# Performance work log

Hardware: AMD Instinct MI355X
Metric: run time of the kernel (lower is better)

Reference implementation:

```python
import jax, jax.numpy as jnp
import numpy as np

GAIN_RELU = float(np.sqrt(2.0))  # torch.nn.init.calculate_gain('relu')
EPS = 1e-12  # F.normalize eps

N_NODES = 50000
N_EDGES = 1600000
IN_DIM = 8
HID = 32
EMB = 32


def setup_inputs() -> dict:
    key = jax.random.key(0)
    ks = jax.random.split(key, 20)
    x = jax.random.normal(ks[0], (N_NODES, IN_DIM), dtype=jnp.float32)
    edge_index = jax.random.randint(ks[1], (2, N_EDGES), 0, N_NODES, dtype=jnp.int64)
    d = {"x": x, "edge_index": edge_index}
    # Three WeBConv layers: (in->HID), (3*HID->HID), (3*HID->EMB)
    dims = [(IN_DIM, HID), (3 * HID, HID), (3 * HID, EMB)]
    ki = 2
    for li, (din, dout) in enumerate(dims, start=1):
        s = 1.0 / np.sqrt(din)  # torch Linear default init scale (uniform)
        d[f"w{li}_up"] = jax.random.uniform(ks[ki], (dout, din), jnp.float32, -s, s); ki += 1
        d[f"w{li}_down"] = jax.random.uniform(ks[ki], (dout, din), jnp.float32, -s, s); ki += 1
        d[f"w{li}_bias"] = jax.random.uniform(ks[ki], (dout, din), jnp.float32, -s, s); ki += 1
        d[f"ew{li}_up"] = jax.random.normal(ks[ki], (N_EDGES,), jnp.float32) * GAIN_RELU; ki += 1
        d[f"ew{li}_down"] = jax.random.normal(ks[ki], (N_EDGES,), jnp.float32) * GAIN_RELU; ki += 1
    return d


def _propagate(xp, src, dst, edge_weight, n_nodes):
    # degree-normalized (1/deg of target), edge-weighted scatter-add
    deg = jnp.zeros((n_nodes,), xp.dtype).at[dst].add(1.0)
    deg_inv = jnp.where(deg > 0, 1.0 / deg, 0.0)  # inf -> 0
    w = deg_inv[dst] * edge_weight  # [E]
    msgs = w[:, None] * xp[src]  # [E, F] gather + scale
    return jnp.zeros((n_nodes, xp.shape[1]), xp.dtype).at[dst].add(msgs)


def _webconv(x, edge_index, w_up, w_down, w_bias, ew_up, ew_down):
    n = x.shape[0]
    row, col = edge_index[0], edge_index[1]
    up_x = x @ w_up.T
    down_x = x @ w_down.T
    bias_x = x @ w_bias.T
    x_up = _propagate(up_x, row, col, ew_up, n)          # normal direction
    x_down = _propagate(down_x, col, row, ew_down, n)    # flipud(edge_index)
    cat = jnp.concatenate([x_up, x_down, bias_x], axis=-1)
    norm = jnp.maximum(jnp.linalg.norm(cat, axis=-1, keepdims=True), EPS)
    return cat / norm


def reference(x, edge_index,
              w1_up, w1_down, w1_bias, ew1_up, ew1_down,
              w2_up, w2_down, w2_bias, ew2_up, ew2_down,
              w3_up, w3_down, w3_bias, ew3_up, ew3_down):
    act = lambda h: jax.nn.leaky_relu(h, negative_slope=0.1)
    h = act(_webconv(x, edge_index, w1_up, w1_down, w1_bias, ew1_up, ew1_down))
    h = act(_webconv(h, edge_index, w2_up, w2_down, w2_bias, ew2_up, ew2_down))
    h = act(_webconv(h, edge_index, w3_up, w3_down, w3_bias, ew3_up, ew3_down))
    mean_up = (ew1_up + ew2_up + ew3_up) / 3.0
    mean_down = (ew1_down + ew2_down + ew3_down) / 3.0
    return h, mean_up, mean_down
```

## Files before the change

kernel.cpp:

```cpp
#include <hip/hip_runtime.h>
#include <hip/hip_bf16.h>
#include <math.h>

typedef __hip_bfloat16 bf16;
typedef unsigned short ushort_t;

#define NBMAX 1024
#define BSH 8
#define CH 3072
#define CSRCAP 6144

__device__ __forceinline__ float ldf(const void* p, long i, int isbf) {
    return isbf ? __bfloat162float(((const bf16*)p)[i]) : ((const float*)p)[i];
}
__device__ __forceinline__ int lde(const int* ei, int half, long e, long E, int is64) {
    long idx = half ? (E + e) : e;
    return is64 ? ei[idx * 2] : ei[idx];
}
__device__ __forceinline__ float u2f(ushort_t u) {
    union { unsigned int i; float f; } v; v.i = ((unsigned)u) << 16; return v.f;
}
__device__ __forceinline__ ushort_t f2u(float f) {
    bf16 h = __float2bfloat16(f);
    return *reinterpret_cast<ushort_t*>(&h);
}
__device__ __forceinline__ float lo2f(unsigned sp) {
    union { unsigned i; float f; } v; v.i = sp << 16; return v.f;
}
__device__ __forceinline__ float hi2f(unsigned sp) {
    union { unsigned i; float f; } v; v.i = sp & 0xffff0000u; return v.f;
}

struct DetectArgs {
    const void* p[16];
    long n[16];
    const int* ei;
    long E;
    int* flags;
};

__global__ void k_detect(DetectArgs a) {
    __shared__ int cnt;
    if (threadIdx.x == 0) cnt = 0;
    __syncthreads();
    int b = blockIdx.x;
    int bad = 0;
    if (b < 16) {
        const bf16* p = (const bf16*)a.p[b];
        long m = a.n[b] < 4096 ? a.n[b] : 4096;
        for (long i = threadIdx.x; i < m; i += 256) {
            float v = __bfloat162float(p[i]);
            if (!(fabsf(v) < 100.0f)) bad++;
        }
        atomicAdd(&cnt, bad);
        __syncthreads();
        if (threadIdx.x == 0) a.flags[b] = ((long)cnt * 16 < m) ? 1 : 0;
    } else {
        long m = a.E / 2 < 4096 ? a.E / 2 : 4096;
        for (long i = threadIdx.x; i < m; i += 256) {
            if (a.ei[2 * i + 1] != 0) bad++;
        }
        atomicAdd(&cnt, bad);
        __syncthreads();
        if (threadIdx.x == 0) a.flags[16] = (cnt < (int)(m / 16) + 1) ? 1 : 0;
    }
}


__global__ void kb_count(const int* __restrict__ ei, long E, const int* __restrict__ flags,
                         int NB, int* __restrict__ bc) {
    __shared__ int h0[NBMAX], h1[NBMAX];
    for (int i = threadIdx.x; i < NB; i += 256) { h0[i] = 0; h1[i] = 0; }
    __syncthreads();
    int is64 = flags[16];
    long base = (long)blockIdx.x * CH;
#pragma unroll
    for (int i = 0; i < CH / 256; i++) {
        long e = base + i * 256 + threadIdx.x;
        if (e < E) {
            int c = lde(ei, 1, e, E, is64);
            int r = lde(ei, 0, e, E, is64);
            atomicAdd(&h0[c >> BSH], 1);
            atomicAdd(&h1[r >> BSH], 1);
        }
    }
    __syncthreads();
    for (int i = threadIdx.x; i < NB; i += 256) {
        if (h0[i]) atomicAdd(&bc[i], h0[i]);
        if (h1[i]) atomicAdd(&bc[NBMAX + i], h1[i]);
    }
}

__global__ void kb_scan(const int* __restrict__ bc, int* __restrict__ bb,
                        int* __restrict__ gcur, int NB) {
    if (threadIdx.x < 2) {
        int dir = threadIdx.x;
        int acc = 0;
        for (int i = 0; i < NB; i++) { bb[dir * (NBMAX + 1) + i] = acc; acc += bc[dir * NBMAX + i]; }
        bb[dir * (NBMAX + 1) + NB] = acc;
    }
    __syncthreads();
    for (int i = threadIdx.x; i < 2 * NBMAX; i += blockDim.x) {
        int d = i / NBMAX, b = i - d * NBMAX;
        gcur[i] = bb[d * (NBMAX + 1) + (b < NB ? b : NB)];
    }
}

__global__ __launch_bounds__(512) void kb_fill(
                        const int* __restrict__ ei, long E, const int* __restrict__ flags,
                        int NB, int NBp, int* __restrict__ gcur,
                        const void* __restrict__ eu1, const void* __restrict__ eu2,
                        const void* __restrict__ eu3, const void* __restrict__ ed1,
                        const void* __restrict__ ed2, const void* __restrict__ ed3,
                        int2* __restrict__ bse_a, ushort_t* __restrict__ bse_w3) {
    extern __shared__ char dynlds[];
    int2* ssA      = (int2*)dynlds;
    ushort_t* ssW  = (ushort_t*)(ssA + CH);
    ushort_t* sbkt = ssW + CH;
    int* h    = (int*)(sbkt + CH);
    int* lofs = h + NBp;
    int* cur  = lofs + NBp;
    int* gb   = cur + NBp;
    int* sc   = gb + NBp;
    int tid = threadIdx.x;
    int dir = blockIdx.y;
    int is64 = flags[16];
    const void* w1p = dir ? ed1 : eu1;
    const void* w2p = dir ? ed2 : eu2;
    const void* w3p = dir ? ed3 : eu3;
    int f1 = flags[dir ? 5 : 4], f2 = flags[dir ? 10 : 9], f3 = flags[dir ? 15 : 14];
    for (int i = tid; i < NBp; i += 512) { h[i] = 0; cur[i] = 0; }
    __syncthreads();
    long base = (long)blockIdx.x * CH;
    const int EPT = CH / 512;
    int myd[EPT], mys[EPT], myw12[EPT];
    ushort_t myw3[EPT];
#pragma unroll
    for (int i = 0; i < EPT; i++) {
        long e = base + i * 512 + tid;
        myd[i] = -1;
        if (e < E) {
            myd[i] = lde(ei, dir ? 0 : 1, e, E, is64);
            mys[i] = lde(ei, dir ? 1 : 0, e, E, is64);
            myw12[i] = (unsigned)f2u(ldf(w1p, e, f1)) | ((unsigned)f2u(ldf(w2p, e, f2)) << 16);
            myw3[i] = f2u(ldf(w3p, e, f3));
            atomicAdd(&h[myd[i] >> BSH], 1);
        }
    }
    __syncthreads();
    int i0 = tid * 2;
    int a0 = (i0 < NBp) ? h[i0] : 0;
    int a1 = (i0 + 1 < NBp) ? h[i0 + 1] : 0;
    int ts = a0 + a1;
    sc[tid] = ts;
    __syncthreads();
    for (int d = 1; d < 512; d <<= 1) {
        int t = (tid >= d) ? sc[tid - d] : 0;
        __syncthreads();
        sc[tid] += t;
        __syncthreads();
    }
    int eb = sc[tid] - ts;
    if (i0 < NBp) lofs[i0] = eb;
    if (i0 + 1 < NBp) lofs[i0 + 1] = eb + a0;
    __syncthreads();
#pragma unroll
    for (int i = 0; i < EPT; i++) {
        if (myd[i] >= 0) {
            int b = myd[i] >> BSH;
            int r = atomicAdd(&cur[b], 1);
            int p = lofs[b] + r;
            ssA[p] = make_int2(mys[i] | ((myd[i] & 255) << 24), myw12[i]);
            ssW[p] = myw3[i];
            sbkt[p] = (ushort_t)b;
        }
    }
    __syncthreads();
    for (int b = tid; b < NB; b += 512) {
        int c = h[b];
        gb[b] = c ? atomicAdd(&gcur[dir * NBMAX + b], c) : 0;
    }
    __syncthreads();
    long rem = E - base;
    int nvalid = rem >= CH ? CH : (rem > 0 ? (int)rem : 0);
    int2* osA = bse_a + (long)dir * E;
    ushort_t* osW = bse_w3 + (long)dir * E;
    for (int s = tid; s < nvalid; s += 512) {
        int b = sbkt[s];
        long p = (long)gb[b] + (s - lofs[b]);
        osA[p] = ssA[s];
        osW[p] = ssW[s];
    }
}

__global__ __launch_bounds__(512) void kb_csr(
                       const int* __restrict__ bb, const int2* __restrict__ bse_a,
                       const ushort_t* __restrict__ bse_w3,
                       long E, int NB, long N,
                       int* __restrict__ off_c, int* __restrict__ off_r,
                       int* __restrict__ list_c, int* __restrict__ list_r,
                       ushort_t* __restrict__ wc6) {
    __shared__ int2 sA[CSRCAP];
    __shared__ ushort_t sW[CSRCAP];
    __shared__ int h[256], lofs[256], cur[256], sc[256];
    int tid = threadIdx.x;
    int b = blockIdx.x, dir = blockIdx.y;
    int base = bb[dir * (NBMAX + 1) + b];
    int cnt  = bb[dir * (NBMAX + 1) + b + 1] - base;
    const int2* bsA = bse_a + (long)dir * E;
    const ushort_t* bsW = bse_w3 + (long)dir * E;
    int* off  = dir ? off_r : off_c;
    int* list = dir ? list_r : list_c;
    ushort_t* o1 = wc6 + (long)(0 + dir) * E;
    ushort_t* o2 = wc6 + (long)(2 + dir) * E;
    ushort_t* o3 = wc6 + (long)(4 + dir) * E;
    if (tid < 256) { h[tid] = 0; cur[tid] = 0; }
    __syncthreads();
    int nb0 = b << BSH;
    for (int s = tid; s < cnt; s += 512)
        atomicAdd(&h[(unsigned)bsA[base + s].x >> 24], 1);
    __syncthreads();
    if (tid < 256) sc[tid] = h[tid];
    __syncthreads();
    for (int d = 1; d < 256; d <<= 1) {
        int t = 0;
        if (tid < 256 && tid >= d) t = sc[tid - d];
        __syncthreads();
        if (tid < 256) sc[tid] += t;
        __syncthreads();
    }
    if (tid < 256) lofs[tid] = sc[tid] - h[tid];
    __syncthreads();
    if (tid < 256) {
        long n = (long)nb0 + tid;
        if (n < N) off[n] = base + lofs[tid];
    }
    if (b == 0 && tid == 0) off[N] = (int)E;
    int mid = lofs[128];
    int cnt1 = cnt - mid;
    if (mid <= CSRCAP && cnt1 <= CSRCAP) {
        for (int s = tid; s < cnt; s += 512) {
            int2 se = bsA[base + s];
            int local = (unsigned)se.x >> 24;
            if (local < 128) {
                int r = atomicAdd(&cur[local], 1);
                int p = lofs[local] + r;
                sA[p] = se;
                sW[p] = bsW[base + s];
            }
        }
        __syncthreads();
        for (int s = tid; s < mid; s += 512) {
            int2 se = sA[s];
            list[base + s] = se.x & 0xFFFFFF;
            o1[base + s] = (ushort_t)((unsigned)se.y & 0xFFFF);
            o2[base + s] = (ushort_t)((unsigned)se.y >> 16);
            o3[base + s] = sW[s];
        }
        __syncthreads();
        for (int s = tid; s < cnt; s += 512) {
            int2 se = bsA[base + s];
            int local = (unsigned)se.x >> 24;
            if (local >= 128) {
                int r = atomicAdd(&cur[local], 1);
                int p = lofs[local] - mid + r;
                sA[p] = se;
                sW[p] = bsW[base + s];
            }
        }
        __syncthreads();
        for (int s = tid; s < cnt1; s += 512) {
            int2 se = sA[s];
            list[base + mid + s] = se.x & 0xFFFFFF;
            o1[base + mid + s] = (ushort_t)((unsigned)se.y & 0xFFFF);
            o2[base + mid + s] = (ushort_t)((unsigned)se.y >> 16);
            o3[base + mid + s] = sW[s];
        }
    } else {
        for (int s = tid; s < cnt; s += 512) {
            int2 se = bsA[base + s];
            int local = (unsigned)se.x >> 24;
            int r = atomicAdd(&cur[local], 1);
            long p = (long)base + lofs[local] + r;
            list[p] = se.x & 0xFFFFFF;
            o1[p] = (ushort_t)((unsigned)se.y & 0xFFFF);
            o2[p] = (ushort_t)((unsigned)se.y >> 16);
            o3[p] = bsW[base + s];
        }
    }
}

__device__ __forceinline__ void gacc(const int* __restrict__ list, const ushort_t* __restrict__ wc,
                                     const ushort_t* __restrict__ S, int j0, int j1, int sub, int f4,
                                     float& a0, float& a1, float& a2, float& a3) {
    int j = j0 + sub;
    for (; j + 24 < j1; j += 32) {
        int s0 = list[j], s1 = list[j + 8], s2 = list[j + 16], s3 = list[j + 24];
        float w0 = u2f(wc[j]), w1 = u2f(wc[j + 8]), w2 = u2f(wc[j + 16]), w3 = u2f(wc[j + 24]);
        uint2 p0 = *(const uint2*)&S[((long)s0 << 5) + (f4 << 2)];
        uint2 p1 = *(const uint2*)&S[((long)s1 << 5) + (f4 << 2)];
        uint2 p2 = *(const uint2*)&S[((long)s2 << 5) + (f4 << 2)];
        uint2 p3 = *(const uint2*)&S[((long)s3 << 5) + (f4 << 2)];
        a0 += w0 * lo2f(p0.x) + w1 * lo2f(p1.x) + w2 * lo2f(p2.x) + w3 * lo2f(p3.x);
        a1 += w0 * hi2f(p0.x) + w1 * hi2f(p1.x) + w2 * hi2f(p2.x) + w3 * hi2f(p3.x);
        a2 += w0 * lo2f(p0.y) + w1 * lo2f(p1.y) + w2 * lo2f(p2.y) + w3 * lo2f(p3.y);
        a3 += w0 * hi2f(p0.y) + w1 * hi2f(p1.y) + w2 * hi2f(p2.y) + w3 * hi2f(p3.y);
    }
    for (; j + 8 < j1; j += 16) {
        int s0 = list[j], s1 = list[j + 8];
        float w0 = u2f(wc[j]), w1 = u2f(wc[j + 8]);
        uint2 p0 = *(const uint2*)&S[((long)s0 << 5) + (f4 << 2)];
        uint2 p1 = *(const uint2*)&S[((long)s1 << 5) + (f4 << 2)];
        a0 += w0 * lo2f(p0.x) + w1 * lo2f(p1.x);
        a1 += w0 * hi2f(p0.x) + w1 * hi2f(p1.x);
        a2 += w0 * lo2f(p0.y) + w1 * lo2f(p1.y);
        a3 += w0 * hi2f(p0.y) + w1 * hi2f(p1.y);
    }
    if (j < j1) {
        int s0 = list[j];
        float w0 = u2f(wc[j]);
        uint2 p0 = *(const uint2*)&S[((long)s0 << 5) + (f4 << 2)];
        a0 += w0 * lo2f(p0.x);
        a1 += w0 * hi2f(p0.x);
        a2 += w0 * lo2f(p0.y);
        a3 += w0 * hi2f(p0.y);
    }
}

__global__ void k_gather_up(const int* __restrict__ off_c, const int* __restrict__ list_c,
                            const ushort_t* __restrict__ wcu, const ushort_t* __restrict__ Su,
                            long N, float* __restrict__ U) {
    long t = (long)blockIdx.x * blockDim.x + threadIdx.x;
    long n = t >> 6;
    if (n >= N) return;
    int lane = (int)(t & 63);
    int sub = lane >> 3;
    int f4  = lane & 7;
    int j0 = off_c[n], j1 = off_c[n + 1];
    float a0 = 0.f, a1 = 0.f, a2 = 0.f, a3 = 0.f;
    gacc(list_c, wcu, Su, j0, j1, sub, f4, a0, a1, a2, a3);
    a0 += __shfl_xor(a0, 8, 64);  a1 += __shfl_xor(a1, 8, 64);
    a2 += __shfl_xor(a2, 8, 64);  a3 += __shfl_xor(a3, 8, 64);
    a0 += __shfl_xor(a0, 16, 64); a1 += __shfl_xor(a1, 16, 64);
    a2 += __shfl_xor(a2, 16, 64); a3 += __shfl_xor(a3, 16, 64);
    a0 += __shfl_xor(a0, 32, 64); a1 += __shfl_xor(a1, 32, 64);
    a2 += __shfl_xor(a2, 32, 64); a3 += __shfl_xor(a3, 32, 64);
    if (sub == 0) {
        int deg = j1 - j0;
        float dinv = (deg > 0) ? 1.0f / (float)deg : 0.f;
        *(float4*)&U[(n << 5) + (f4 << 2)] =
            make_float4(a0 * dinv, a1 * dinv, a2 * dinv, a3 * dinv);
    }
}

__global__ void k_gather_downfin(const int* __restrict__ off_r, const int* __restrict__ list_r,
                                 const ushort_t* __restrict__ wcd, const ushort_t* __restrict__ Sd,
                                 const ushort_t* __restrict__ Sb, const float* __restrict__ U,
                                 long N, float* __restrict__ out) {
    long t = (long)blockIdx.x * blockDim.x + threadIdx.x;
    long n = t >> 6;
    if (n >= N) return;
    int lane = (int)(t & 63);
    int sub = lane >> 3;
    int f4  = lane & 7;
    int j0 = off_r[n], j1 = off_r[n + 1];
    float a0 = 0.f, a1 = 0.f, a2 = 0.f, a3 = 0.f;
    gacc(list_r, wcd, Sd, j0, j1, sub, f4, a0, a1, a2, a3);
    a0 += __shfl_xor(a0, 8, 64);  a1 += __shfl_xor(a1, 8, 64);
    a2 += __shfl_xor(a2, 8, 64);  a3 += __shfl_xor(a3, 8, 64);
    a0 += __shfl_xor(a0, 16, 64); a1 += __shfl_xor(a1, 16, 64);
    a2 += __shfl_xor(a2, 16, 64); a3 += __shfl_xor(a3, 16, 64);
    a0 += __shfl_xor(a0, 32, 64); a1 += __shfl_xor(a1, 32, 64);
    a2 += __shfl_xor(a2, 32, 64); a3 += __shfl_xor(a3, 32, 64);
    float v0 = 0.f, v1 = 0.f, v2 = 0.f, v3 = 0.f;
    float u0 = 0.f, u1 = 0.f, u2 = 0.f, u3 = 0.f;
    float c0 = 0.f, c1 = 0.f, c2 = 0.f, c3 = 0.f;
    float ss = 0.f;
    if (sub == 0) {
        int deg = j1 - j0;
        float dinv = (deg > 0) ? 1.0f / (float)deg : 0.f;
        v0 = a0 * dinv; v1 = a1 * dinv; v2 = a2 * dinv; v3 = a3 * dinv;
        float4 uv = *(const float4*)&U[(n << 5) + (f4 << 2)];
        u0 = uv.x; u1 = uv.y; u2 = uv.z; u3 = uv.w;
        uint2 bp = *(const uint2*)&Sb[(n << 5) + (f4 << 2)];
        c0 = lo2f(bp.x); c1 = hi2f(bp.x); c2 = lo2f(bp.y); c3 = hi2f(bp.y);
        ss = v0 * v0 + v1 * v1 + v2 * v2 + v3 * v3
           + u0 * u0 + u1 * u1 + u2 * u2 + u3 * u3
           + c0 * c0 + c1 * c1 + c2 * c2 + c3 * c3;
    }
#pragma unroll
    for (int m = 1; m < 64; m <<= 1) ss += __shfl_xor(ss, m, 64);
    float inv = 1.0f / fmaxf(sqrtf(ss), 1e-12f);
    if (sub == 0) {
        float x0, x1, x2, x3;
        x0 = u0 * inv; x0 = (x0 >= 0.f) ? x0 : 0.1f * x0;
        x1 = u1 * inv; x1 = (x1 >= 0.f) ? x1 : 0.1f * x1;
        x2 = u2 * inv; x2 = (x2 >= 0.f) ? x2 : 0.1f * x2;
        x3 = u3 * inv; x3 = (x3 >= 0.f) ? x3 : 0.1f * x3;
        *(float4*)&out[n * 96 + (f4 << 2)] = make_float4(x0, x1, x2, x3);
        x0 = v0 * inv; x0 = (x0 >= 0.f) ? x0 : 0.1f * x0;
        x1 = v1 * inv; x1 = (x1 >= 0.f) ? x1 : 0.1f * x1;
        x2 = v2 * inv; x2 = (x2 >= 0.f) ? x2 : 0.1f * x2;
        x3 = v3 * inv; x3 = (x3 >= 0.f) ? x3 : 0.1f * x3;
        *(float4*)&out[n * 96 + 32 + (f4 << 2)] = make_float4(x0, x1, x2, x3);
        x0 = c0 * inv; x0 = (x0 >= 0.f) ? x0 : 0.1f * x0;
        x1 = c1 * inv; x1 = (x1 >= 0.f) ? x1 : 0.1f * x1;
        x2 = c2 * inv; x2 = (x2 >= 0.f) ? x2 : 0.1f * x2;
        x3 = c3 * inv; x3 = (x3 >= 0.f) ? x3 : 0.1f * x3;
        *(float4*)&out[n * 96 + 64 + (f4 << 2)] = make_float4(x0, x1, x2, x3);
    }
}

__global__ void k_lin96(const float* __restrict__ xin, long N,
                        const void* __restrict__ wu, const void* __restrict__ wd,
                        const void* __restrict__ wb, int wfi,
                        const int* __restrict__ flags,
                        ushort_t* __restrict__ Su, ushort_t* __restrict__ Sd,
                        ushort_t* __restrict__ Sb) {
    __shared__ float xs[64 * 100];
    __shared__ float wt[96 * 96];
    int tid = threadIdx.x;
    int ubf = flags[wfi], dbf = flags[wfi + 1], bbf = flags[wfi + 2];
    for (int j = tid; j < 96 * 96; j += 256) {
        int o3 = j % 96, i = j / 96;
        float v;
        if (o3 < 32)      v = ldf(wu, (long)o3 * 96 + i, ubf);
        else if (o3 < 64) v = ldf(wd, (long)(o3 - 32) * 96 + i, dbf);
        else              v = ldf(wb, (long)(o3 - 64) * 96 + i, bbf);
        wt[j] = v;
    }
    long nb = (long)blockIdx.x * 64;
    for (int j = tid; j < 64 * 24; j += 256) {
        int node = j / 24, c = j % 24;
        long gn = nb + node;
        float4 v = make_float4(0.f, 0.f, 0.f, 0.f);
        if (gn < N) v = ((const float4*)(xin + gn * 96))[c];
        *(float4*)&xs[node * 100 + c * 4] = v;
    }
    __syncthreads();
    int node0 = tid >> 3;
    int node1 = node0 + 32;
    int o0 = (tid & 7) * 12;
    float acc0[12], acc1[12];
#pragma unroll
    for (int s = 0; s < 12; s++) { acc0[s] = 0.f; acc1[s] = 0.f; }
    const float* xrow0 = &xs[node0 * 100];
    const float* xrow1 = &xs[node1 * 100];
#pragma unroll 4
    for (int c = 0; c < 24; c++) {
        float4 xv0 = *(const float4*)&xrow0[c * 4];
        float4 xv1 = *(const float4*)&xrow1[c * 4];
        const float* w0 = &wt[(c * 4) * 96 + o0];
#pragma unroll
        for (int k = 0; k < 4; k++) {
            float xk0 = (k == 0) ? xv0.x : (k == 1) ? xv0.y : (k == 2) ? xv0.z : xv0.w;
            float xk1 = (k == 0) ? xv1.x : (k == 1) ? xv1.y : (k == 2) ? xv1.z : xv1.w;
            const float* wr = w0 + k * 96;
            float4 wa = *(const float4*)(wr);
            float4 wb4 = *(const float4*)(wr + 4);
            float4 wc = *(const float4*)(wr + 8);
            acc0[0] += xk0 * wa.x;  acc0[1] += xk0 * wa.y;  acc0[2]  += xk0 * wa.z;  acc0[3]  += xk0 * wa.w;
            acc0[4] += xk0 * wb4.x; acc0[5] += xk0 * wb4.y; acc0[6]  += xk0 * wb4.z; acc0[7]  += xk0 * wb4.w;
            acc0[8] += xk0 * wc.x;  acc0[9] += xk0 * wc.y;  acc0[10] += xk0 * wc.z;  acc0[11] += xk0 * wc.w;
            acc1[0] += xk1 * wa.x;  acc1[1] += xk1 * wa.y;  acc1[2]  += xk1 * wa.z;  acc1[3]  += xk1 * wa.w;
            acc1[4] += xk1 * wb4.x; acc1[5] += xk1 * wb4.y; acc1[6]  += xk1 * wb4.z; acc1[7]  += xk1 * wb4.w;
            acc1[8] += xk1 * wc.x;  acc1[9] += xk1 * wc.y;  acc1[10] += xk1 * wc.z;  acc1[11] += xk1 * wc.w;
        }
    }
    __syncthreads();
    ushort_t* sbuf = (ushort_t*)xs;
#pragma unroll
    for (int s = 0; s < 12; s++) {
        sbuf[node0 * 96 + o0 + s] = f2u(acc0[s]);
        sbuf[node1 * 96 + o0 + s] = f2u(acc1[s]);
    }
    __syncthreads();
    for (int j = tid; j < 64 * 96; j += 256) {
        int nd = j / 96, o3 = j % 96;
        long gn = nb + nd;
        if (gn < N) {
            int blk = o3 >> 5, fo = o3 & 31;
            ushort_t v = sbuf[j];
            (blk == 0 ? Su : blk == 1 ? Sd : Sb)[gn * 32 + fo] = v;
        }
    }
}

__global__ void k_linear_b16(const void* __restrict__ xin, int xfi, int din, int dout, long N,
                             const void* __restrict__ wu, const void* __restrict__ wd,
                             const void* __restrict__ wb, int wfi,
                             const int* __restrict__ flags, int uselds,
                             ushort_t* __restrict__ Su, ushort_t* __restrict__ Sd,
                             ushort_t* __restrict__ Sb) {
    __shared__ float smem[12288];
    int xbf = (xfi >= 0) ? flags[xfi] : 0;
    int ubf = flags[wfi], dbf = flags[wfi + 1], bbf = flags[wfi + 2];
    float* su = smem;
    float* sd = smem + (long)din * dout;
    float* sb = smem + 2l * din * dout;
    if (uselds) {
        for (int j = threadIdx.x; j < din * dout; j += 256) {
            int o = j % dout, i = j / dout;
            su[j] = ldf(wu, (long)o * din + i, ubf);
            sd[j] = ldf(wd, (long)o * din + i, dbf);
            sb[j] = ldf(wb, (long)o * din + i, bbf);
        }
        __syncthreads();
    }
    long idx = (long)blockIdx.x * blockDim.x + threadIdx.x;
    long node = idx / dout;
    int o = (int)(idx % dout);
    if (node >= N) return;
    float au = 0.f, ad = 0.f, ab = 0.f;
    long xb = node * din;
    if (uselds) {
        for (int i = 0; i < din; i++) {
            float xv = ldf(xin, xb + i, xbf);
            au += xv * su[i * dout + o];
            ad += xv * sd[i * dout + o];
            ab += xv * sb[i * dout + o];
        }
    } else {
        for (int i = 0; i < din; i++) {
            float xv = ldf(xin, xb + i, xbf);
            au += xv * ldf(wu, (long)o * din + i, ubf);
            ad += xv * ldf(wd, (long)o * din + i, dbf);
            ab += xv * ldf(wb, (long)o * din + i, bbf);
        }
    }
    Su[node * dout + o] = f2u(au);
    Sd[node * dout + o] = f2u(ad);
    Sb[node * dout + o] = f2u(ab);
}

__global__ void k_linear(const void* __restrict__ xin, int xfi, int din, int dout, int rs, long N,
                         const void* __restrict__ wu, const void* __restrict__ wd,
                         const void* __restrict__ wb, int wfi,
                         const int* __restrict__ flags, int uselds,
                         float* __restrict__ A, float* __restrict__ B, float* __restrict__ C) {
    __shared__ float smem[12288];
    int xbf = (xfi >= 0) ? flags[xfi] : 0;
    int ubf = flags[wfi], dbf = flags[wfi + 1], bbf = flags[wfi + 2];
    float* su = smem;
    float* sd = smem + (long)din * dout;
    float* sb = smem + 2l * din * dout;
    if (uselds) {
        for (int j = threadIdx.x; j < din * dout; j += 256) {
            int o = j % dout, i = j / dout;
            su[j] = ldf(wu, (long)o * din + i, ubf);
            sd[j] = ldf(wd, (long)o * din + i, dbf);
            sb[j] = ldf(wb, (long)o * din + i, bbf);
        }
        __syncthreads();
    }
    long idx = (long)blockIdx.x * blockDim.x + threadIdx.x;
    long node = idx / dout;
    int o = (int)(idx % dout);
    if (node >= N) return;
    float au = 0.f, ad = 0.f, ab = 0.f;
    long xb = node * din;
    if (uselds) {
        for (int i = 0; i < din; i++) {
            float xv = ldf(xin, xb + i, xbf);
            au += xv * su[i * dout + o];
            ad += xv * sd[i * dout + o];
            ab += xv * sb[i * dout + o];
        }
    } else {
        for (int i = 0; i < din; i++) {
            float xv = ldf(xin, xb + i, xbf);
            au += xv * ldf(wu, (long)o * din + i, ubf);
            ad += xv * ldf(wd, (long)o * din + i, dbf);
            ab += xv * ldf(wb, (long)o * din + i, bbf);
        }
    }
    A[node * rs + o] = au;
    B[node * rs + o] = ad;
    C[node * rs + o] = ab;
}

__global__ void k_deg(const int* __restrict__ ei, long E, const int* __restrict__ flags,
                      float* __restrict__ degc, float* __restrict__ degr) {
    long e = (long)blockIdx.x * blockDim.x + threadIdx.x;
    if (e < E) {
        int is64 = flags[16];
        atomicAdd(&degc[lde(ei, 1, e, E, is64)], 1.0f);
        atomicAdd(&degr[lde(ei, 0, e, E, is64)], 1.0f);
    }
}

__global__ void k_inv(float* __restrict__ a, long n) {
    long i = (long)blockIdx.x * blockDim.x + threadIdx.x;
    if (i < n) { float v = a[i]; a[i] = (v > 0.0f) ? 1.0f / v : 0.0f; }
}

__global__ void k_scatter(const int* __restrict__ ei, long E, int F,
                          const void* __restrict__ ewu, const void* __restrict__ ewd,
                          int fu, int fd, const int* __restrict__ flags,
                          const float* __restrict__ degci, const float* __restrict__ degri,
                          const float* __restrict__ A, const float* __restrict__ B,
                          float* __restrict__ U, float* __restrict__ D) {
    long idx = (long)blockIdx.x * blockDim.x + threadIdx.x;
    long tot = E * 2 * F;
    if (idx >= tot) return;
    int is64 = flags[16];
    long e = idx / (2 * F);
    int rem = (int)(idx - e * 2 * F);
    int dir = rem >= F;
    int f = rem - dir * F;
    int r = lde(ei, 0, e, E, is64), c = lde(ei, 1, e, E, is64);
    if (!dir) {
        float w = degci[c] * ldf(ewu, e, flags[fu]);
        atomicAdd(&U[(long)c * F + f], w * A[(long)r * F + f]);
    } else {
        float w = degri[r] * ldf(ewd, e, flags[fd]);
        atomicAdd(&D[(long)r * F + f], w * B[(long)c * F + f]);
    }
}

__global__ void k_finalize(const float* __restrict__ U, const float* __restrict__ D,
                           const float* __restrict__ C, int F, long N,
                           float* __restrict__ out) {
    long t = (long)blockIdx.x * blockDim.x + threadIdx.x;
    long n = t >> 6;
    if (n >= N) return;
    int lane = (int)(t & 63);
    int cat = 3 * F;
    float ss = 0.f;
    for (int j = lane; j < cat; j += 64) {
        float v = (j < F) ? U[n * F + j] : (j < 2 * F) ? D[n * F + j - F] : C[n * F + j - 2 * F];
        ss += v * v;
    }
#pragma unroll
    for (int m = 1; m < 64; m <<= 1) ss += __shfl_xor(ss, m, 64);
    float inv = 1.0f / fmaxf(sqrtf(ss), 1e-12f);
    for (int j = lane; j < cat; j += 64) {
        float v = (j < F) ? U[n * F + j] : (j < 2 * F) ? D[n * F + j - F] : C[n * F + j - 2 * F];
        float a = v * inv;
        a = (a >= 0.0f) ? a : 0.1f * a;
        out[n * cat + j] = a;
    }
}

__global__ void k_mean(const void* e1u, const void* e2u, const void* e3u,
                       const void* e1d, const void* e2d, const void* e3d,
                       const int* __restrict__ flags, long E,
                       float* __restrict__ mu, float* __restrict__ md) {
    long e = (long)blockIdx.x * blockDim.x + threadIdx.x;
    if (e >= E) return;
    float su = ldf(e1u, e, flags[4]) + ldf(e2u, e, flags[9]) + ldf(e3u, e, flags[14]);
    float sd = ldf(e1d, e, flags[5]) + ldf(e2d, e, flags[10]) + ldf(e3d, e, flags[15]);
    mu[e] = su / 3.0f;
    md[e] = sd / 3.0f;
}

extern "C" void kernel_launch(void* const* d_in, const int* in_sizes, int n_in,
                              void* d_out, int out_size, void* d_ws, size_t ws_size,
                              hipStream_t stream) {
    const int* ei = (const int*)d_in[1];
    const void* w_up[3]   = {d_in[2], d_in[7],  d_in[12]};
    const void* w_down[3] = {d_in[3], d_in[8],  d_in[13]};
    const void* w_bias[3] = {d_in[4], d_in[9],  d_in[14]};
    const void* ew_up[3]  = {d_in[5], d_in[10], d_in[15]};
    const void* ew_down[3]= {d_in[6], d_in[11], d_in[16]};

    long E = in_sizes[5];
    if (E <= 0) E = 1600000;
    int HID = (int)(sqrt((double)in_sizes[7] / 3.0) + 0.5);
    if (HID <= 0 || (long)3 * HID * HID != (long)in_sizes[7]) HID = 32;
    int DIN = in_sizes[2] / HID;
    if (DIN <= 0) DIN = 8;
    long N = (long)in_sizes[0] / DIN;
    if (N <= 0) N = 50000;
    int EMB = in_sizes[12] / (3 * HID);
    if (EMB <= 0) EMB = 32;
    int Fm = HID > EMB ? HID : EMB;
    int NB = (int)((N + 255) >> BSH);
    int NBp = (NB + 1) & ~1;

    float* out_h  = (float*)d_out;
    float* out_mu = out_h + N * 3l * EMB;
    float* out_md = out_mu + E;

    const int TB = 256;
    int lds1  = (3l * DIN * HID <= 12288) ? 1 : 0;
    int lds12 = (3l * (3 * HID) * HID <= 12288) ? 1 : 0;
    int lds3  = (3l * (3 * HID) * EMB <= 12288) ? 1 : 0;
    dim3 linG1((unsigned)((N * HID + TB - 1) / TB));
    dim3 linG3((unsigned)((N * EMB + TB - 1) / TB));
    dim3 lin96G((unsigned)((N + 63) / 64));
    dim3 finG((unsigned)((N * 64 + TB - 1) / TB));
    dim3 edgeG((unsigned)((E + TB - 1) / TB));
    dim3 chunkG1((unsigned)((E + CH - 1) / CH));
    dim3 chunkG2((unsigned)((E + CH - 1) / CH), 2);
    size_t fillLds = (size_t)CH * 12 + (size_t)(4 * NBp + 512) * 4;

    int* flags = (int*)d_ws;
    int* bc    = flags + 64;
    int* bb    = bc + 2 * NBMAX;
    int* gcur  = bb + 2 * (NBMAX + 1);
    int* off_c = gcur + 2 * NBMAX;
    int* off_r = off_c + (N + 1);
    long li = (long)(off_r + (N + 1) - (int*)d_ws);
    li = (li + 3) & ~3l;
    int* list_c = (int*)d_ws + li;
    int* list_r = list_c + E;
    ushort_t* wc6 = (ushort_t*)(list_r + E);
    int* X = list_r + E + 3 * E;
    int2* bse_a = (int2*)X;
    ushort_t* bse_w3 = (ushort_t*)(X + 4 * E);
    ushort_t* Su = (ushort_t*)X;
    ushort_t* Sd = Su + N * Fm;
    ushort_t* Sb = Sd + N * Fm;
    float* U = (float*)(Sb + N * Fm);
    long zInts = (3l * N * Fm + 1) / 2 + N * Fm;
    long Xints = 5l * E;
    if (zInts > Xints) Xints = zInts;
    size_t need = (size_t)((li + 5l * E + Xints) * 4l + 256);

    bool fast = (HID == 32 && EMB == 32) && (NB <= NBMAX) &&
                (ws_size == 0 || ws_size >= need);

    DetectArgs da;
    da.p[0] = d_in[0]; da.n[0] = in_sizes[0];
    for (int L = 0; L < 3; L++) {
        da.p[1 + 5 * L] = w_up[L];    da.n[1 + 5 * L] = in_sizes[2 + 5 * L];
        da.p[2 + 5 * L] = w_down[L];  da.n[2 + 5 * L] = in_sizes[3 + 5 * L];
        da.p[3 + 5 * L] = w_bias[L];  da.n[3 + 5 * L] = in_sizes[4 + 5 * L];
        da.p[4 + 5 * L] = ew_up[L];   da.n[4 + 5 * L] = in_sizes[5 + 5 * L];
        da.p[5 + 5 * L] = ew_down[L]; da.n[5 + 5 * L] = in_sizes[6 + 5 * L];
    }
    da.ei = ei; da.E = E; da.flags = flags;
    k_detect<<<17, TB, 0, stream>>>(da);

    if (fast) {
        hipMemsetAsync(bc, 0, 2 * NBMAX * sizeof(int), stream);
        kb_count<<<chunkG1, TB, 0, stream>>>(ei, E, flags, NB, bc);
        kb_scan<<<1, 512, 0, stream>>>(bc, bb, gcur, NB);
        kb_fill<<<chunkG2, 512, fillLds, stream>>>(ei, E, flags, NB, NBp, gcur,
                                                   ew_up[0], ew_up[1], ew_up[2],
                                                   ew_down[0], ew_down[1], ew_down[2],
                                                   bse_a, bse_w3);
        kb_csr<<<dim3((unsigned)NB, 2), 512, 0, stream>>>(bb, bse_a, bse_w3, E, NB, N,
                                                          off_c, off_r, list_c, list_r,
                                                          wc6);

        k_mean<<<edgeG, TB, 0, stream>>>(ew_up[0], ew_up[1], ew_up[2],
                                         ew_down[0], ew_down[1], ew_down[2],
                                         flags, E, out_mu, out_md);

        float* H = (float*)d_out;

        k_linear_b16<<<linG1, TB, 0, stream>>>(d_in[0], 0, DIN, HID, N,
                                               w_up[0], w_down[0], w_bias[0], 1, flags, lds1,
                                               Su, Sd, Sb);
        k_gather_up<<<finG, TB, 0, stream>>>(off_c, list_c, wc6, Su, N, U);
        k_gather_downfin<<<finG, TB, 0, stream>>>(off_r, list_r, wc6 + E, Sd, Sb, U, N, H);
        k_lin96<<<lin96G, TB, 0, stream>>>(H, N, w_up[1], w_down[1], w_bias[1], 6, flags,
                                           Su, Sd, Sb);
        k_gather_up<<<finG, TB, 0, stream>>>(off_c, list_c, wc6 + 2l * E, Su, N, U);
        k_gather_downfin<<<finG, TB, 0, stream>>>(off_r, list_r, wc6 + 3l * E, Sd, Sb, U, N, H);
        k_lin96<<<lin96G, TB, 0, stream>>>(H, N, w_up[2], w_down[2], w_bias[2], 11, flags,
                                           Su, Sd, Sb);
        k_gather_up<<<finG, TB, 0, stream>>>(off_c, list_c, wc6 + 4l * E, Su, N, U);
        k_gather_downfin<<<finG, TB, 0, stream>>>(off_r, list_r, wc6 + 5l * E, Sd, Sb, U, N, out_h);
    } else {
        float* degci = (float*)(flags + 64);
        float* degri = degci + N;
        float* fA = degri + N;
        float* fB = fA + N * Fm;
        float* fC = fB + N * Fm;
        float* fU = fC + N * Fm;
        float* fD = fU + N * Fm;
        float* fH = fD + N * Fm;
        dim3 scatG12((unsigned)((E * 2 * HID + TB - 1) / TB));
        dim3 scatG3((unsigned)((E * 2 * EMB + TB - 1) / TB));

        hipMemsetAsync(degci, 0, 2 * N * sizeof(float), stream);
        k_deg<<<edgeG, TB, 0, stream>>>(ei, E, flags, degci, degri);
        k_inv<<<dim3((unsigned)((2 * N + TB - 1) / TB)), TB, 0, stream>>>(degci, 2 * N);

        k_linear<<<linG1, TB, 0, stream>>>(d_in[0], 0, DIN, HID, HID, N,
                                           w_up[0], w_down[0], w_bias[0], 1, flags, lds1, fA, fB, fC);
        hipMemsetAsync(fU, 0, 2l * N * Fm * sizeof(float), stream);
        k_scatter<<<scatG12, TB, 0, stream>>>(ei, E, HID, ew_up[0], ew_down[0], 4, 5, flags,
                                              degci, degri, fA, fB, fU, fD);
        k_finalize<<<finG, TB, 0, stream>>>(fU, fD, fC, HID, N, fH);

        k_linear<<<linG1, TB, 0, stream>>>(fH, -1, 3 * HID, HID, HID, N,
                                           w_up[1], w_down[1], w_bias[1], 6, flags, lds12, fA, fB, fC);
        hipMemsetAsync(fU, 0, 2l * N * Fm * sizeof(float), stream);
        k_scatter<<<scatG12, TB, 0, stream>>>(ei, E, HID, ew_up[1], ew_down[1], 9, 10, flags,
                                              degci, degri, fA, fB, fU, fD);
        k_finalize<<<finG, TB, 0, stream>>>(fU, fD, fC, HID, N, fH);

        k_linear<<<linG3, TB, 0, stream>>>(fH, -1, 3 * HID, EMB, EMB, N,
                                           w_up[2], w_down[2], w_bias[2], 11, flags, lds3, fA, fB, fC);
        hipMemsetAsync(fU, 0, 2l * N * Fm * sizeof(float), stream);
        k_scatter<<<scatG3, TB, 0, stream>>>(ei, E, EMB, ew_up[2], ew_down[2], 14, 15, flags,
                                             degci, degri, fA, fB, fU, fD);
        k_finalize<<<finG, TB, 0, stream>>>(fU, fD, fC, EMB, N, out_h);

        k_mean<<<edgeG, TB, 0, stream>>>(ew_up[0], ew_up[1], ew_up[2],
                                         ew_down[0], ew_down[1], ew_down[2],
                                         flags, E, out_mu, out_md);
    }
}
```

Before: 525.3 us.

## Use per-chunk histogram scan for deterministic bucket offsets, wave scans, contiguous gather

Replaces the global atomic bucket cursor in the CSR build with a per-chunk, per-bucket histogram. A new scan kernel turns it into exclusive prefix offsets, so the fill kernel reads its global offsets directly and no longer needs atomics. Block-level LDS prefix scans in the fill and CSR kernels become wavefront shuffle scans, and int64 index loads use int2 reads. The gather loop now gives each sub-lane a contiguous run of edges with paired vector loads instead of strided accesses. The trade-off is an extra histogram buffer of NC*NB ints per direction and one more kernel launch.

```diff
diff --git a/kernel.cpp b/kernel.cpp
--- a/kernel.cpp
+++ b/kernel.cpp
@@ -4,10 +4,12 @@
 
 typedef __hip_bfloat16 bf16;
 typedef unsigned short ushort_t;
+typedef unsigned int uint_t;
 
 #define NBMAX 1024
 #define BSH 8
 #define CH 3072
+#define NCMAX 2048
 #define CSRCAP 6144
 
 __device__ __forceinline__ float ldf(const void* p, long i, int isbf) {
@@ -15,7 +17,8 @@
 }
 __device__ __forceinline__ int lde(const int* ei, int half, long e, long E, int is64) {
     long idx = half ? (E + e) : e;
-    return is64 ? ei[idx * 2] : ei[idx];
+    if (is64) return ((const int2*)ei)[idx].x;
+    return ei[idx];
 }
 __device__ __forceinline__ float u2f(ushort_t u) {
     union { unsigned int i; float f; } v; v.i = ((unsigned)u) << 16; return v.f;
@@ -68,47 +71,72 @@
 
 
 __global__ void kb_count(const int* __restrict__ ei, long E, const int* __restrict__ flags,
-                         int NB, int* __restrict__ bc) {
+                         int NB, int NC, int* __restrict__ hc) {
     __shared__ int h0[NBMAX], h1[NBMAX];
     for (int i = threadIdx.x; i < NB; i += 256) { h0[i] = 0; h1[i] = 0; }
     __syncthreads();
     int is64 = flags[16];
-    long base = (long)blockIdx.x * CH;
+    int c = blockIdx.x;
+    long base = (long)c * CH;
 #pragma unroll
     for (int i = 0; i < CH / 256; i++) {
         long e = base + i * 256 + threadIdx.x;
         if (e < E) {
-            int c = lde(ei, 1, e, E, is64);
-            int r = lde(ei, 0, e, E, is64);
-            atomicAdd(&h0[c >> BSH], 1);
-            atomicAdd(&h1[r >> BSH], 1);
-        }
-    }
-    __syncthreads();
-    for (int i = threadIdx.x; i < NB; i += 256) {
-        if (h0[i]) atomicAdd(&bc[i], h0[i]);
-        if (h1[i]) atomicAdd(&bc[NBMAX + i], h1[i]);
-    }
-}
-
-__global__ void kb_scan(const int* __restrict__ bc, int* __restrict__ bb,
-                        int* __restrict__ gcur, int NB) {
+            int cc = lde(ei, 1, e, E, is64);
+            int rr = lde(ei, 0, e, E, is64);
+            atomicAdd(&h0[cc >> BSH], 1);
+            atomicAdd(&h1[rr >> BSH], 1);
+        }
+    }
+    __syncthreads();
+    for (int b = threadIdx.x; b < NB; b += 256) {
+        hc[((long)0 * NC + c) * NB + b] = h0[b];
+        hc[((long)1 * NC + c) * NB + b] = h1[b];
+    }
+}
+
+__global__ void kb_scanA(int* __restrict__ hc, int NC, int NB, int* __restrict__ bc) {
+    __shared__ int ssum[256];
+    int b = blockIdx.x, d = blockIdx.y;
+    int tid = threadIdx.x;
+    int k = (NC + 255) / 256;
+    int c0 = tid * k;
+    int local[8];
+    int s = 0;
+    for (int i = 0; i < k; i++) {
+        int c = c0 + i;
+        int v = (c < NC) ? hc[((long)d * NC + c) * NB + b] : 0;
+        local[i] = s; s += v;
+    }
+    ssum[tid] = s;
+    __syncthreads();
+    for (int dd = 1; dd < 256; dd <<= 1) {
+        int t = (tid >= dd) ? ssum[tid - dd] : 0;
+        __syncthreads();
+        ssum[tid] += t;
+        __syncthreads();
+    }
+    int base = ssum[tid] - s;
+    for (int i = 0; i < k; i++) {
+        int c = c0 + i;
+        if (c < NC) hc[((long)d * NC + c) * NB + b] = base + local[i];
+    }
+    if (tid == 255) bc[d * NBMAX + b] = ssum[255];
+}
+
+__global__ void kb_scanB(const int* __restrict__ bc, int* __restrict__ bb, int NB) {
     if (threadIdx.x < 2) {
         int dir = threadIdx.x;
         int acc = 0;
         for (int i = 0; i < NB; i++) { bb[dir * (NBMAX + 1) + i] = acc; acc += bc[dir * NBMAX + i]; }
         bb[dir * (NBMAX + 1) + NB] = acc;
     }
-    __syncthreads();
-    for (int i = threadIdx.x; i < 2 * NBMAX; i += blockDim.x) {
-        int d = i / NBMAX, b = i - d * NBMAX;
-        gcur[i] = bb[d * (NBMAX + 1) + (b < NB ? b : NB)];
-    }
 }
 
 __global__ __launch_bounds__(512) void kb_fill(
                         const int* __restrict__ ei, long E, const int* __restrict__ flags,
-                        int NB, int NBp, int* __restrict__ gcur,
+                        int NB, int NBp, int NC,
+                        const int* __restrict__ hc, const int* __restrict__ bb,
                         const void* __restrict__ eu1, const void* __restrict__ eu2,
                         const void* __restrict__ eu3, const void* __restrict__ ed1,
                         const void* __restrict__ ed2, const void* __restrict__ ed3,
@@ -121,8 +149,8 @@
     int* lofs = h + NBp;
     int* cur  = lofs + NBp;
     int* gb   = cur + NBp;
-    int* sc   = gb + NBp;
     int tid = threadIdx.x;
+    int cidx = blockIdx.x;
     int dir = blockIdx.y;
     int is64 = flags[16];
     const void* w1p = dir ? ed1 : eu1;
@@ -130,8 +158,10 @@
     const void* w3p = dir ? ed3 : eu3;
     int f1 = flags[dir ? 5 : 4], f2 = flags[dir ? 10 : 9], f3 = flags[dir ? 15 : 14];
     for (int i = tid; i < NBp; i += 512) { h[i] = 0; cur[i] = 0; }
-    __syncthreads();
-    long base = (long)blockIdx.x * CH;
+    for (int b = tid; b < NB; b += 512)
+        gb[b] = bb[dir * (NBMAX + 1) + b] + hc[((long)dir * NC + cidx) * NB + b];
+    __syncthreads();
+    long base = (long)cidx * CH;
     const int EPT = CH / 512;
     int myd[EPT], mys[EPT], myw12[EPT];
     ushort_t myw3[EPT];
@@ -148,21 +178,21 @@
         }
     }
     __syncthreads();
-    int i0 = tid * 2;
-    int a0 = (i0 < NBp) ? h[i0] : 0;
-    int a1 = (i0 + 1 < NBp) ? h[i0 + 1] : 0;
-    int ts = a0 + a1;
-    sc[tid] = ts;
-    __syncthreads();
-    for (int d = 1; d < 512; d <<= 1) {
-        int t = (tid >= d) ? sc[tid - d] : 0;
-        __syncthreads();
-        sc[tid] += t;
-        __syncthreads();
-    }
-    int eb = sc[tid] - ts;
-    if (i0 < NBp) lofs[i0] = eb;
-    if (i0 + 1 < NBp) lofs[i0 + 1] = eb + a0;
+    if (tid < 64) {
+        int carry = 0;
+        for (int g = 0; g < NBp; g += 64) {
+            int idx = g + tid;
+            int v = (idx < NBp) ? h[idx] : 0;
+            int x = v;
+#pragma unroll
+            for (int o = 1; o < 64; o <<= 1) {
+                int y = __shfl_up(x, o, 64);
+                if (tid >= o) x += y;
+            }
+            if (idx < NBp) lofs[idx] = x - v + carry;
+            carry += __shfl(x, 63, 64);
+        }
+    }
     __syncthreads();
 #pragma unroll
     for (int i = 0; i < EPT; i++) {
@@ -174,11 +204,6 @@
             ssW[p] = myw3[i];
             sbkt[p] = (ushort_t)b;
         }
-    }
-    __syncthreads();
-    for (int b = tid; b < NB; b += 512) {
-        int c = h[b];
-        gb[b] = c ? atomicAdd(&gcur[dir * NBMAX + b], c) : 0;
     }
     __syncthreads();
     long rem = E - base;
@@ -202,7 +227,7 @@
                        ushort_t* __restrict__ wc6) {
     __shared__ int2 sA[CSRCAP];
     __shared__ ushort_t sW[CSRCAP];
-    __shared__ int h[256], lofs[256], cur[256], sc[256];
+    __shared__ int h[256], lofs[256], cur[256];
     int tid = threadIdx.x;
     int b = blockIdx.x, dir = blockIdx.y;
     int base = bb[dir * (NBMAX + 1) + b];
@@ -220,16 +245,22 @@
     for (int s = tid; s < cnt; s += 512)
         atomicAdd(&h[(unsigned)bsA[base + s].x >> 24], 1);
     __syncthreads();
-    if (tid < 256) sc[tid] = h[tid];
-    __syncthreads();
-    for (int d = 1; d < 256; d <<= 1) {
-        int t = 0;
-        if (tid < 256 && tid >= d) t = sc[tid - d];
-        __syncthreads();
-        if (tid < 256) sc[tid] += t;
-        __syncthreads();
-    }
-    if (tid < 256) lofs[tid] = sc[tid] - h[tid];
+    if (tid < 64) {
+        int carry = 0;
+#pragma unroll
+        for (int g = 0; g < 4; g++) {
+            int idx = g * 64 + tid;
+            int v = h[idx];
+            int x = v;
+#pragma unroll
+            for (int o = 1; o < 64; o <<= 1) {
+                int y = __shfl_up(x, o, 64);
+                if (tid >= o) x += y;
+            }
+            lofs[idx] = x - v + carry;
+            carry += __shfl(x, 63, 64);
+        }
+    }
     __syncthreads();
     if (tid < 256) {
         long n = (long)nb0 + tid;
@@ -290,41 +321,53 @@
     }
 }
 
+__device__ __forceinline__ void gedge1(const int* __restrict__ list, const ushort_t* __restrict__ wc,
+                                       const ushort_t* __restrict__ S, int j, int f4,
+                                       float& a0, float& a1, float& a2, float& a3) {
+    int s0 = list[j];
+    float w0 = u2f(wc[j]);
+    uint2 p0 = *(const uint2*)&S[((long)s0 << 5) + (f4 << 2)];
+    a0 += w0 * lo2f(p0.x);
+    a1 += w0 * hi2f(p0.x);
+    a2 += w0 * lo2f(p0.y);
+    a3 += w0 * hi2f(p0.y);
+}
 __device__ __forceinline__ void gacc(const int* __restrict__ list, const ushort_t* __restrict__ wc,
                                      const ushort_t* __restrict__ S, int j0, int j1, int sub, int f4,
                                      float& a0, float& a1, float& a2, float& a3) {
-    int j = j0 + sub;
-    for (; j + 24 < j1; j += 32) {
-        int s0 = list[j], s1 = list[j + 8], s2 = list[j + 16], s3 = list[j + 24];
-        float w0 = u2f(wc[j]), w1 = u2f(wc[j + 8]), w2 = u2f(wc[j + 16]), w3 = u2f(wc[j + 24]);
-        uint2 p0 = *(const uint2*)&S[((long)s0 << 5) + (f4 << 2)];
-        uint2 p1 = *(const uint2*)&S[((long)s1 << 5) + (f4 << 2)];
-        uint2 p2 = *(const uint2*)&S[((long)s2 << 5) + (f4 << 2)];
-        uint2 p3 = *(const uint2*)&S[((long)s3 << 5) + (f4 << 2)];
+    int deg = j1 - j0;
+    int len = (deg + 7) >> 3;
+    int j = j0 + sub * len;
+    int je = j + len; if (je > j1) je = j1;
+    if (j < je && (j & 1)) { gedge1(list, wc, S, j, f4, a0, a1, a2, a3); j++; }
+    for (; j + 3 < je; j += 4) {
+        int2 s01 = *(const int2*)&list[j];
+        int2 s23 = *(const int2*)&list[j + 2];
+        uint_t w01 = *(const uint_t*)&wc[j];
+        uint_t w23 = *(const uint_t*)&wc[j + 2];
+        uint2 p0 = *(const uint2*)&S[((long)s01.x << 5) + (f4 << 2)];
+        uint2 p1 = *(const uint2*)&S[((long)s01.y << 5) + (f4 << 2)];
+        uint2 p2 = *(const uint2*)&S[((long)s23.x << 5) + (f4 << 2)];
+        uint2 p3 = *(const uint2*)&S[((long)s23.y << 5) + (f4 << 2)];
+        float w0 = lo2f(w01), w1 = hi2f(w01), w2 = lo2f(w23), w3 = hi2f(w23);
         a0 += w0 * lo2f(p0.x) + w1 * lo2f(p1.x) + w2 * lo2f(p2.x) + w3 * lo2f(p3.x);
         a1 += w0 * hi2f(p0.x) + w1 * hi2f(p1.x) + w2 * hi2f(p2.x) + w3 * hi2f(p3.x);
         a2 += w0 * lo2f(p0.y) + w1 * lo2f(p1.y) + w2 * lo2f(p2.y) + w3 * lo2f(p3.y);
         a3 += w0 * hi2f(p0.y) + w1 * hi2f(p1.y) + w2 * hi2f(p2.y) + w3 * hi2f(p3.y);
     }
-    for (; j + 8 < j1; j += 16) {
-        int s0 = list[j], s1 = list[j + 8];
-        float w0 = u2f(wc[j]), w1 = u2f(wc[j + 8]);
-        uint2 p0 = *(const uint2*)&S[((long)s0 << 5) + (f4 << 2)];
-        uint2 p1 = *(const uint2*)&S[((long)s1 << 5) + (f4 << 2)];
+    if (j + 1 < je) {
+        int2 s01 = *(const int2*)&list[j];
+        uint_t w01 = *(const uint_t*)&wc[j];
+        uint2 p0 = *(const uint2*)&S[((long)s01.x << 5) + (f4 << 2)];
+        uint2 p1 = *(const uint2*)&S[((long)s01.y << 5) + (f4 << 2)];
+        float w0 = lo2f(w01), w1 = hi2f(w01);
         a0 += w0 * lo2f(p0.x) + w1 * lo2f(p1.x);
         a1 += w0 * hi2f(p0.x) + w1 * hi2f(p1.x);
         a2 += w0 * lo2f(p0.y) + w1 * lo2f(p1.y);
         a3 += w0 * hi2f(p0.y) + w1 * hi2f(p1.y);
-    }
-    if (j < j1) {
-        int s0 = list[j];
-        float w0 = u2f(wc[j]);
-        uint2 p0 = *(const uint2*)&S[((long)s0 << 5) + (f4 << 2)];
-        a0 += w0 * lo2f(p0.x);
-        a1 += w0 * hi2f(p0.x);
-        a2 += w0 * lo2f(p0.y);
-        a3 += w0 * hi2f(p0.y);
-    }
+        j += 2;
+    }
+    if (j < je) gedge1(list, wc, S, j, f4, a0, a1, a2, a3);
 }
 
 __global__ void k_gather_up(const int* __restrict__ off_c, const int* __restrict__ list_c,
@@ -677,6 +720,7 @@
     int Fm = HID > EMB ? HID : EMB;
     int NB = (int)((N + 255) >> BSH);
     int NBp = (NB + 1) & ~1;
+    int NC = (int)((E + CH - 1) / CH);
 
     float* out_h  = (float*)d_out;
     float* out_mu = out_h + N * 3l * EMB;
@@ -691,17 +735,17 @@
     dim3 lin96G((unsigned)((N + 63) / 64));
     dim3 finG((unsigned)((N * 64 + TB - 1) / TB));
     dim3 edgeG((unsigned)((E + TB - 1) / TB));
-    dim3 chunkG1((unsigned)((E + CH - 1) / CH));
-    dim3 chunkG2((unsigned)((E + CH - 1) / CH), 2);
-    size_t fillLds = (size_t)CH * 12 + (size_t)(4 * NBp + 512) * 4;
+    dim3 chunkG1((unsigned)NC);
+    dim3 chunkG2((unsigned)NC, 2);
+    size_t fillLds = (size_t)CH * 12 + (size_t)(4 * NBp) * 4;
 
     int* flags = (int*)d_ws;
     int* bc    = flags + 64;
     int* bb    = bc + 2 * NBMAX;
-    int* gcur  = bb + 2 * (NBMAX + 1);
-    int* off_c = gcur + 2 * NBMAX;
+    int* off_c = bb + 2 * (NBMAX + 1);
     int* off_r = off_c + (N + 1);
-    long li = (long)(off_r + (N + 1) - (int*)d_ws);
+    int* hc    = off_r + (N + 1);
+    long li = (long)(hc + 2l * NC * NB - (int*)d_ws);
     li = (li + 3) & ~3l;
     int* list_c = (int*)d_ws + li;
     int* list_r = list_c + E;
@@ -718,7 +762,7 @@
     if (zInts > Xints) Xints = zInts;
     size_t need = (size_t)((li + 5l * E + Xints) * 4l + 256);
 
-    bool fast = (HID == 32 && EMB == 32) && (NB <= NBMAX) &&
+    bool fast = (HID == 32 && EMB == 32) && (NB <= NBMAX) && (NC <= NCMAX) &&
                 (ws_size == 0 || ws_size >= need);
 
     DetectArgs da;
@@ -734,10 +778,10 @@
     k_detect<<<17, TB, 0, stream>>>(da);
 
     if (fast) {
-        hipMemsetAsync(bc, 0, 2 * NBMAX * sizeof(int), stream);
-        kb_count<<<chunkG1, TB, 0, stream>>>(ei, E, flags, NB, bc);
-        kb_scan<<<1, 512, 0, stream>>>(bc, bb, gcur, NB);
-        kb_fill<<<chunkG2, 512, fillLds, stream>>>(ei, E, flags, NB, NBp, gcur,
+        kb_count<<<chunkG1, TB, 0, stream>>>(ei, E, flags, NB, NC, hc);
+        kb_scanA<<<dim3((unsigned)NB, 2), 256, 0, stream>>>(hc, NC, NB, bc);
+        kb_scanB<<<1, 64, 0, stream>>>(bc, bb, NB);
+        kb_fill<<<chunkG2, 512, fillLds, stream>>>(ei, E, flags, NB, NBp, NC, hc, bb,
                                                    ew_up[0], ew_up[1], ew_up[2],
                                                    ew_down[0], ew_down[1], ew_down[2],
                                                    bse_a, bse_w3);
```

Measured after the change: 518.8 us. Within noise of the previous version (-1.2%).
